# Performance work log

Hardware: AMD Instinct MI355X
Metric: run time of the kernel (lower is better)

## Reference

```python
import jax, jax.numpy as jnp
import numpy as np

VAR_W = 1.0
DIST_W = 1.0
M_VAR = 0.1
M_DIST = 1.5
IGNORE = 255
C = 16  # static upper bound on instance ids (labels 1..C; 0 = background)


def setup_inputs() -> dict:
    key = jax.random.key(0)
    ks = jax.random.split(key, 6)
    shapes = [(16, 1, 1024, 1024), (16, 1, 512, 512), (16, 1, 256, 256)]
    d = {}
    for idx, s in enumerate(shapes):
        d[f"featmap{idx}"] = jax.random.normal(ks[idx], s, dtype=jnp.float32)
        d[f"gt{idx}"] = jax.random.randint(ks[3 + idx], s, 0, C + 1, dtype=jnp.int32)
    return d


def _push_pull(feats, gts):
    B = feats[0].shape[0]
    nseg = B * (C + 1)
    b_off = (jnp.arange(B, dtype=jnp.int32) * (C + 1))[:, None]  # [B,1]

    segs, valids, ffs = [], [], []
    tot_sum = jnp.zeros((nseg,), dtype=feats[0].dtype)
    tot_cnt = jnp.zeros((nseg,), dtype=feats[0].dtype)
    # pass 1: per (batch, instance) sums / counts pooled over all scales
    for f, g in zip(feats, gts):
        ff = f.reshape(B, -1)            # [B, N_s]
        gg = g.reshape(B, -1)
        valid = (gg >= 1) & (gg <= C) & (gg < IGNORE)
        lab = jnp.where(valid, gg, 0)
        seg = (lab + b_off).reshape(-1)  # [B*N_s], segment id = b*(C+1)+label
        vf = valid.reshape(-1).astype(ff.dtype)
        tot_sum = tot_sum + jax.ops.segment_sum(jnp.where(valid, ff, 0.0).reshape(-1), seg, num_segments=nseg)
        tot_cnt = tot_cnt + jax.ops.segment_sum(vf, seg, num_segments=nseg)
        segs.append(seg); valids.append(valid); ffs.append(ff)

    mean = tot_sum / jnp.maximum(tot_cnt, 1.0)  # [nseg] per-(b,instance) mean over all scales

    # pass 2: pull loss -- per-scale mean of clamp(|x - mean| - margin_var, 0)^2, summed over scales
    pull_seg = jnp.zeros((nseg,), dtype=feats[0].dtype)
    for ff, seg, valid in zip(ffs, segs, valids):
        m_pix = mean[seg].reshape(ff.shape)
        val = jnp.where(valid, jnp.square(jnp.maximum(jnp.abs(ff - m_pix) - M_VAR, 0.0)), 0.0)
        ssum = jax.ops.segment_sum(val.reshape(-1), seg, num_segments=nseg)
        scnt = jax.ops.segment_sum(valid.reshape(-1).astype(ff.dtype), seg, num_segments=nseg)
        pull_seg = pull_seg + jnp.where(scnt > 0, ssum / jnp.maximum(scnt, 1.0), 0.0)

    present = tot_cnt.reshape(B, C + 1)[:, 1:] > 0        # [B,C]
    pull_i = pull_seg.reshape(B, C + 1)[:, 1:]            # [B,C]
    n_pull = jnp.maximum(present.sum(), 1).astype(pull_i.dtype)
    pull_loss = jnp.sum(jnp.where(present, pull_i, 0.0)) / n_pull * VAR_W

    # push loss: all ordered pairs (i,j), i!=j, both present in that batch element
    m = mean.reshape(B, C + 1)[:, 1:]                     # [B,C]
    diff = jnp.abs(m[:, :, None] - m[:, None, :])         # [B,C,C]
    pv = jnp.square(jnp.maximum(2.0 * M_DIST - diff, 0.0))
    pm = present[:, :, None] & present[:, None, :] & ~jnp.eye(C, dtype=bool)[None]
    n_push = jnp.maximum(pm.sum(), 1).astype(pv.dtype)
    push_loss = jnp.sum(jnp.where(pm, pv, 0.0)) / n_push * DIST_W

    return push_loss + pull_loss


def reference(featmap0, featmap1, featmap2, gt0, gt1, gt2):
    return _push_pull([featmap0, featmap1, featmap2], [gt0, gt1, gt2])
```

## Files before the change

kernel.cpp:

```cpp
#include <hip/hip_runtime.h>


#define NSEG 272
#define M_VAR 0.1f
#define TWO_M_DIST 3.0f

__device__ __forceinline__ void gatomic_add(float* p, float v) {
  __hip_atomic_fetch_add(p, v, __ATOMIC_RELAXED, __HIP_MEMORY_SCOPE_AGENT);
}

#define GRID_BLOCKS 1008

struct Sel {
  const float4* f; const int4* g;
  int vbase, vend, stride, scale, batch;
};

__device__ __forceinline__ Sel pick(
    int b, int t,
    const float4* f0, const int4* g0,
    const float4* f1, const int4* g1,
    const float4* f2, const int4* g2) {
  Sel s;
  if (b < 768) {
    int batch = b / 48, sub = b - batch * 48;
    s.f = f0; s.g = g0; s.scale = 0; s.batch = batch;
    s.vbase = batch * 262144 + sub * 256 + t;
    s.vend  = (batch + 1) * 262144;
    s.stride = 48 * 256;
  } else if (b < 960) {
    int lb = b - 768; int batch = lb / 12, sub = lb - batch * 12;
    s.f = f1; s.g = g1; s.scale = 1; s.batch = batch;
    s.vbase = batch * 65536 + sub * 256 + t;
    s.vend  = (batch + 1) * 65536;
    s.stride = 12 * 256;
  } else {
    int lb = b - 960; int batch = lb / 3, sub = lb - batch * 3;
    s.f = f2; s.g = g2; s.scale = 2; s.batch = batch;
    s.vbase = batch * 16384 + sub * 256 + t;
    s.vend  = (batch + 1) * 16384;
    s.stride = 3 * 256;
  }
  return s;
}

__global__ __launch_bounds__(256, 4) void pass1_kernel(
    const float4* __restrict__ f0, const int4* __restrict__ g0,
    const float4* __restrict__ f1, const int4* __restrict__ g1,
    const float4* __restrict__ f2, const int4* __restrict__ g2,
    float* __restrict__ tot_sum,
    float* __restrict__ cnt)
{
  __shared__ float2 bins[17 * 256];
  const int t = threadIdx.x;
  for (int i = t; i < 17 * 256; i += 256) bins[i] = make_float2(0.f, 0.f);
  __syncthreads();

  Sel s = pick(blockIdx.x, t, f0, g0, f1, g1, f2, g2);

  for (int v = s.vbase; v < s.vend; v += s.stride) {
    float4 fv = s.f[v];
    int4   gv = s.g[v];
    {
      int idx = (int)min((unsigned)gv.x, 16u) * 256 + t;
      float2 r = bins[idx]; bins[idx] = make_float2(r.x + fv.x, r.y + 1.f);
    }
    {
      int idx = (int)min((unsigned)gv.y, 16u) * 256 + t;
      float2 r = bins[idx]; bins[idx] = make_float2(r.x + fv.y, r.y + 1.f);
    }
    {
      int idx = (int)min((unsigned)gv.z, 16u) * 256 + t;
      float2 r = bins[idx]; bins[idx] = make_float2(r.x + fv.z, r.y + 1.f);
    }
    {
      int idx = (int)min((unsigned)gv.w, 16u) * 256 + t;
      float2 r = bins[idx]; bins[idx] = make_float2(r.x + fv.w, r.y + 1.f);
    }
  }

  for (int sh = 7; sh >= 0; --sh) {
    __syncthreads();
    int off = 1 << sh;
    for (int i = t; i < 17 * off; i += 256) {
      int l = i >> sh, tt = i & (off - 1);
      int a = l * 256 + tt;
      float2 x = bins[a], y = bins[a + off];
      bins[a] = make_float2(x.x + y.x, x.y + y.y);
    }
  }
  __syncthreads();

  if (t >= 1 && t < 17) {
    float2 r = bins[t * 256];
    if (r.y != 0.f) {
      gatomic_add(&tot_sum[s.batch * 17 + t], r.x);
      gatomic_add(&cnt[s.scale * NSEG + s.batch * 17 + t], r.y);
    }
  }
}

__global__ __launch_bounds__(256) void mean_kernel(
    const float* __restrict__ tot_sum, const float* __restrict__ cnt,
    float* __restrict__ mean, float* __restrict__ tot_cnt) {
  for (int i = threadIdx.x; i < NSEG; i += 256) {
    float c = cnt[i] + cnt[NSEG + i] + cnt[2 * NSEG + i];
    tot_cnt[i] = c;
    mean[i] = tot_sum[i] / fmaxf(c, 1.f);
  }
}

__global__ __launch_bounds__(256, 8) void pass2_kernel(
    const float4* __restrict__ f0, const int4* __restrict__ g0,
    const float4* __restrict__ f1, const int4* __restrict__ g1,
    const float4* __restrict__ f2, const int4* __restrict__ g2,
    const float* __restrict__ mean,
    float* __restrict__ pull)
{
  __shared__ float bins[17 * 256];
  __shared__ float s_mean[17];
  const int t = threadIdx.x;

  Sel s = pick(blockIdx.x, t, f0, g0, f1, g1, f2, g2);

  for (int i = t; i < 17 * 256; i += 256) bins[i] = 0.f;
  if (t < 17) s_mean[t] = mean[s.batch * 17 + t];
  __syncthreads();

  for (int v = s.vbase; v < s.vend; v += s.stride) {
    float4 fv = s.f[v];
    int4   gv = s.g[v];
    {
      int l = (int)min((unsigned)gv.x, 16u);
      float d = fmaxf(fabsf(fv.x - s_mean[l]) - M_VAR, 0.f);
      bins[l * 256 + t] += d * d;
    }
    {
      int l = (int)min((unsigned)gv.y, 16u);
      float d = fmaxf(fabsf(fv.y - s_mean[l]) - M_VAR, 0.f);
      bins[l * 256 + t] += d * d;
    }
    {
      int l = (int)min((unsigned)gv.z, 16u);
      float d = fmaxf(fabsf(fv.z - s_mean[l]) - M_VAR, 0.f);
      bins[l * 256 + t] += d * d;
    }
    {
      int l = (int)min((unsigned)gv.w, 16u);
      float d = fmaxf(fabsf(fv.w - s_mean[l]) - M_VAR, 0.f);
      bins[l * 256 + t] += d * d;
    }
  }

  for (int sh = 7; sh >= 0; --sh) {
    __syncthreads();
    int off = 1 << sh;
    for (int i = t; i < 17 * off; i += 256) {
      int l = i >> sh, tt = i & (off - 1);
      bins[l * 256 + tt] += bins[l * 256 + tt + off];
    }
  }
  __syncthreads();

  if (t >= 1 && t < 17) {
    float r = bins[t * 256];
    if (r != 0.f) gatomic_add(&pull[s.scale * NSEG + s.batch * 17 + t], r);
  }
}

__global__ __launch_bounds__(256) void finalize_kernel(
    const float* __restrict__ tot_cnt, const float* __restrict__ mean,
    const float* __restrict__ cnt, const float* __restrict__ pull,
    float* __restrict__ out) {
  __shared__ float s_mean[NSEG];
  __shared__ unsigned char s_pres[NSEG];
  const int t = threadIdx.x;
  for (int i = t; i < NSEG; i += 256) {
    s_mean[i] = mean[i];
    s_pres[i] = (tot_cnt[i] > 0.f) ? 1 : 0;
  }
  __syncthreads();

  float pull_v = 0.f, pull_n = 0.f, push_v = 0.f, push_n = 0.f;

  for (int i = t; i < NSEG; i += 256) {
    int lab = i - (i / 17) * 17;
    if (lab >= 1 && s_pres[i]) {
      float ps = 0.f;
      float c0 = cnt[i];            if (c0 > 0.f) ps += pull[i] / c0;
      float c1 = cnt[NSEG + i];     if (c1 > 0.f) ps += pull[NSEG + i] / c1;
      float c2 = cnt[2 * NSEG + i]; if (c2 > 0.f) ps += pull[2 * NSEG + i] / c2;
      pull_v += ps;
      pull_n += 1.f;
    }
  }

  {
    int b = t >> 4, ii = t & 15;
    int si = b * 17 + ii + 1;
    if (s_pres[si]) {
      float mi = s_mean[si];
      for (int j = 0; j < 16; ++j) {
        if (j == ii) continue;
        int sj = b * 17 + j + 1;
        if (s_pres[sj]) {
          float d = fmaxf(TWO_M_DIST - fabsf(mi - s_mean[sj]), 0.f);
          push_v += d * d;
          push_n += 1.f;
        }
      }
    }
  }

  #pragma unroll
  for (int o = 32; o > 0; o >>= 1) {
    pull_v += __shfl_down(pull_v, o);
    pull_n += __shfl_down(pull_n, o);
    push_v += __shfl_down(push_v, o);
    push_n += __shfl_down(push_n, o);
  }
  __shared__ float r[4][4];
  int wave = t >> 6;
  if ((t & 63) == 0) { r[wave][0] = pull_v; r[wave][1] = pull_n; r[wave][2] = push_v; r[wave][3] = push_n; }
  __syncthreads();
  if (t == 0) {
    float PV = 0, PN = 0, SV = 0, SN = 0;
    for (int w = 0; w < 4; ++w) { PV += r[w][0]; PN += r[w][1]; SV += r[w][2]; SN += r[w][3]; }
    out[0] = PV / fmaxf(PN, 1.f) + SV / fmaxf(SN, 1.f);
  }
}

extern "C" void kernel_launch(void* const* d_in, const int* in_sizes, int n_in,
                              void* d_out, int out_size, void* d_ws, size_t ws_size,
                              hipStream_t stream) {
  const float4* f0 = (const float4*)d_in[0];
  const int4*   g0 = (const int4*)  d_in[1];
  const float4* f1 = (const float4*)d_in[2];
  const int4*   g1 = (const int4*)  d_in[3];
  const float4* f2 = (const float4*)d_in[4];
  const int4*   g2 = (const int4*)  d_in[5];

  float* ws      = (float*)d_ws;
  float* tot_sum = ws;
  float* cnt     = ws + NSEG;
  float* pull    = ws + 4 * NSEG;
  float* mean    = ws + 7 * NSEG;
  float* tot_cnt = ws + 8 * NSEG;

  hipMemsetAsync(d_ws, 0, 7 * NSEG * sizeof(float), stream);
  pass1_kernel<<<GRID_BLOCKS, 256, 0, stream>>>(f0, g0, f1, g1, f2, g2, tot_sum, cnt);
  mean_kernel<<<1, 256, 0, stream>>>(tot_sum, cnt, mean, tot_cnt);
  pass2_kernel<<<GRID_BLOCKS, 256, 0, stream>>>(f0, g0, f1, g1, f2, g2, mean, pull);
  finalize_kernel<<<1, 256, 0, stream>>>(tot_cnt, mean, cnt, pull, (float*)d_out);
}
```

Before: 213.9 us.

## Replace LDS histograms with register accumulators and fuse mean/finalize kernels

Both passes now keep one register accumulator per instance label, updated with predicated adds, and reduce them with wave shuffles instead of per-thread LDS bins and a tree reduction. The loop software-prefetches the next float4/int4. The mean kernel is folded into pass2's prologue, and finalize runs in the last block, chosen by an atomic ticket counter. This removes LDS traffic and two launches, at the cost of 16 compare-selects per pixel and more register pressure.

```diff
diff --git a/kernel.cpp b/kernel.cpp
--- a/kernel.cpp
+++ b/kernel.cpp
@@ -4,17 +4,13 @@
 #define NSEG 272
 #define M_VAR 0.1f
 #define TWO_M_DIST 3.0f
+#define GRID_BLOCKS 1008
 
 __device__ __forceinline__ void gatomic_add(float* p, float v) {
   __hip_atomic_fetch_add(p, v, __ATOMIC_RELAXED, __HIP_MEMORY_SCOPE_AGENT);
 }
 
-#define GRID_BLOCKS 1008
-
-struct Sel {
-  const float4* f; const int4* g;
-  int vbase, vend, stride, scale, batch;
-};
+struct Sel { const float4* f; const int4* g; int vbase, vend, stride, scale, batch; };
 
 __device__ __forceinline__ Sel pick(
     int b, int t,
@@ -25,21 +21,15 @@
   if (b < 768) {
     int batch = b / 48, sub = b - batch * 48;
     s.f = f0; s.g = g0; s.scale = 0; s.batch = batch;
-    s.vbase = batch * 262144 + sub * 256 + t;
-    s.vend  = (batch + 1) * 262144;
-    s.stride = 48 * 256;
+    s.vbase = batch * 262144 + sub * 256 + t; s.vend = (batch + 1) * 262144; s.stride = 48 * 256;
   } else if (b < 960) {
-    int lb = b - 768; int batch = lb / 12, sub = lb - batch * 12;
+    int lb = b - 768, batch = lb / 12, sub = lb - batch * 12;
     s.f = f1; s.g = g1; s.scale = 1; s.batch = batch;
-    s.vbase = batch * 65536 + sub * 256 + t;
-    s.vend  = (batch + 1) * 65536;
-    s.stride = 12 * 256;
+    s.vbase = batch * 65536 + sub * 256 + t; s.vend = (batch + 1) * 65536; s.stride = 12 * 256;
   } else {
-    int lb = b - 960; int batch = lb / 3, sub = lb - batch * 3;
+    int lb = b - 960, batch = lb / 3, sub = lb - batch * 3;
     s.f = f2; s.g = g2; s.scale = 2; s.batch = batch;
-    s.vbase = batch * 16384 + sub * 256 + t;
-    s.vend  = (batch + 1) * 16384;
-    s.stride = 3 * 256;
+    s.vbase = batch * 16384 + sub * 256 + t; s.vend = (batch + 1) * 16384; s.stride = 3 * 256;
   }
   return s;
 }
@@ -51,133 +41,140 @@
     float* __restrict__ tot_sum,
     float* __restrict__ cnt)
 {
-  __shared__ float2 bins[17 * 256];
   const int t = threadIdx.x;
-  for (int i = t; i < 17 * 256; i += 256) bins[i] = make_float2(0.f, 0.f);
-  __syncthreads();
-
   Sel s = pick(blockIdx.x, t, f0, g0, f1, g1, f2, g2);
 
-  for (int v = s.vbase; v < s.vend; v += s.stride) {
-    float4 fv = s.f[v];
-    int4   gv = s.g[v];
-    {
-      int idx = (int)min((unsigned)gv.x, 16u) * 256 + t;
-      float2 r = bins[idx]; bins[idx] = make_float2(r.x + fv.x, r.y + 1.f);
-    }
-    {
-      int idx = (int)min((unsigned)gv.y, 16u) * 256 + t;
-      float2 r = bins[idx]; bins[idx] = make_float2(r.x + fv.y, r.y + 1.f);
-    }
-    {
-      int idx = (int)min((unsigned)gv.z, 16u) * 256 + t;
-      float2 r = bins[idx]; bins[idx] = make_float2(r.x + fv.z, r.y + 1.f);
-    }
-    {
-      int idx = (int)min((unsigned)gv.w, 16u) * 256 + t;
-      float2 r = bins[idx]; bins[idx] = make_float2(r.x + fv.w, r.y + 1.f);
-    }
-  }
-
-  for (int sh = 7; sh >= 0; --sh) {
-    __syncthreads();
-    int off = 1 << sh;
-    for (int i = t; i < 17 * off; i += 256) {
-      int l = i >> sh, tt = i & (off - 1);
-      int a = l * 256 + tt;
-      float2 x = bins[a], y = bins[a + off];
-      bins[a] = make_float2(x.x + y.x, x.y + y.y);
-    }
-  }
-  __syncthreads();
-
-  if (t >= 1 && t < 17) {
-    float2 r = bins[t * 256];
-    if (r.y != 0.f) {
-      gatomic_add(&tot_sum[s.batch * 17 + t], r.x);
-      gatomic_add(&cnt[s.scale * NSEG + s.batch * 17 + t], r.y);
-    }
-  }
-}
-
-__global__ __launch_bounds__(256) void mean_kernel(
-    const float* __restrict__ tot_sum, const float* __restrict__ cnt,
-    float* __restrict__ mean, float* __restrict__ tot_cnt) {
-  for (int i = threadIdx.x; i < NSEG; i += 256) {
-    float c = cnt[i] + cnt[NSEG + i] + cnt[2 * NSEG + i];
-    tot_cnt[i] = c;
-    mean[i] = tot_sum[i] / fmaxf(c, 1.f);
-  }
-}
-
-__global__ __launch_bounds__(256, 8) void pass2_kernel(
+  float sum[16]; int cn[16];
+  #pragma unroll
+  for (int l = 0; l < 16; ++l) { sum[l] = 0.f; cn[l] = 0; }
+
+  auto body = [&](float f, int g) {
+    #pragma unroll
+    for (int l = 0; l < 16; ++l) {
+      bool m = (g == l + 1);
+      sum[l] += m ? f : 0.f;
+      cn[l]  += m ? 1 : 0;
+    }
+  };
+
+  int v = s.vbase;
+  bool have = v < s.vend;
+  float4 fv; int4 gv;
+  if (have) { fv = s.f[v]; gv = s.g[v]; }
+  while (have) {
+    int vn = v + s.stride;
+    bool hn = vn < s.vend;
+    float4 fn; int4 gn;
+    if (hn) { fn = s.f[vn]; gn = s.g[vn]; }
+    body(fv.x, gv.x); body(fv.y, gv.y); body(fv.z, gv.z); body(fv.w, gv.w);
+    fv = fn; gv = gn; v = vn; have = hn;
+  }
+
+  #pragma unroll
+  for (int l = 0; l < 16; ++l) {
+    #pragma unroll
+    for (int o = 32; o > 0; o >>= 1) {
+      sum[l] += __shfl_down(sum[l], o);
+      cn[l]  += __shfl_down(cn[l], o);
+    }
+  }
+  __shared__ float rs[4][16];
+  __shared__ int   rc[4][16];
+  int wave = t >> 6, lane = t & 63;
+  if (lane == 0) {
+    #pragma unroll
+    for (int l = 0; l < 16; ++l) { rs[wave][l] = sum[l]; rc[wave][l] = cn[l]; }
+  }
+  __syncthreads();
+  if (t < 16) {
+    float sv = rs[0][t] + rs[1][t] + rs[2][t] + rs[3][t];
+    int   cv = rc[0][t] + rc[1][t] + rc[2][t] + rc[3][t];
+    if (cv != 0) {
+      gatomic_add(&tot_sum[s.batch * 17 + t + 1], sv);
+      gatomic_add(&cnt[s.scale * NSEG + s.batch * 17 + t + 1], (float)cv);
+    }
+  }
+}
+
+__global__ __launch_bounds__(256, 4) void pass2_kernel(
     const float4* __restrict__ f0, const int4* __restrict__ g0,
     const float4* __restrict__ f1, const int4* __restrict__ g1,
     const float4* __restrict__ f2, const int4* __restrict__ g2,
-    const float* __restrict__ mean,
-    float* __restrict__ pull)
+    const float* __restrict__ tot_sum,
+    const float* __restrict__ cnt,
+    float* __restrict__ pull,
+    int* __restrict__ counter,
+    float* __restrict__ out)
 {
-  __shared__ float bins[17 * 256];
   __shared__ float s_mean[17];
   const int t = threadIdx.x;
-
   Sel s = pick(blockIdx.x, t, f0, g0, f1, g1, f2, g2);
 
-  for (int i = t; i < 17 * 256; i += 256) bins[i] = 0.f;
-  if (t < 17) s_mean[t] = mean[s.batch * 17 + t];
-  __syncthreads();
-
-  for (int v = s.vbase; v < s.vend; v += s.stride) {
-    float4 fv = s.f[v];
-    int4   gv = s.g[v];
-    {
-      int l = (int)min((unsigned)gv.x, 16u);
-      float d = fmaxf(fabsf(fv.x - s_mean[l]) - M_VAR, 0.f);
-      bins[l * 256 + t] += d * d;
-    }
-    {
-      int l = (int)min((unsigned)gv.y, 16u);
-      float d = fmaxf(fabsf(fv.y - s_mean[l]) - M_VAR, 0.f);
-      bins[l * 256 + t] += d * d;
-    }
-    {
-      int l = (int)min((unsigned)gv.z, 16u);
-      float d = fmaxf(fabsf(fv.z - s_mean[l]) - M_VAR, 0.f);
-      bins[l * 256 + t] += d * d;
-    }
-    {
-      int l = (int)min((unsigned)gv.w, 16u);
-      float d = fmaxf(fabsf(fv.w - s_mean[l]) - M_VAR, 0.f);
-      bins[l * 256 + t] += d * d;
-    }
-  }
-
-  for (int sh = 7; sh >= 0; --sh) {
-    __syncthreads();
-    int off = 1 << sh;
-    for (int i = t; i < 17 * off; i += 256) {
-      int l = i >> sh, tt = i & (off - 1);
-      bins[l * 256 + tt] += bins[l * 256 + tt + off];
-    }
-  }
-  __syncthreads();
-
-  if (t >= 1 && t < 17) {
-    float r = bins[t * 256];
-    if (r != 0.f) gatomic_add(&pull[s.scale * NSEG + s.batch * 17 + t], r);
-  }
-}
-
-__global__ __launch_bounds__(256) void finalize_kernel(
-    const float* __restrict__ tot_cnt, const float* __restrict__ mean,
-    const float* __restrict__ cnt, const float* __restrict__ pull,
-    float* __restrict__ out) {
-  __shared__ float s_mean[NSEG];
-  __shared__ unsigned char s_pres[NSEG];
-  const int t = threadIdx.x;
+  if (t < 17) {
+    int seg = s.batch * 17 + t;
+    float c = cnt[seg] + cnt[NSEG + seg] + cnt[2 * NSEG + seg];
+    s_mean[t] = tot_sum[seg] / fmaxf(c, 1.f);
+  }
+  __syncthreads();
+
+  float acc[16];
+  #pragma unroll
+  for (int l = 0; l < 16; ++l) acc[l] = 0.f;
+
+  auto body = [&](float f, int g) {
+    unsigned gi = (unsigned)g; gi = gi > 16u ? 16u : gi;
+    float d = fmaxf(fabsf(f - s_mean[gi]) - M_VAR, 0.f);
+    float d2 = d * d;
+    #pragma unroll
+    for (int l = 0; l < 16; ++l) acc[l] += (g == l + 1) ? d2 : 0.f;
+  };
+
+  int v = s.vbase;
+  bool have = v < s.vend;
+  float4 fv; int4 gv;
+  if (have) { fv = s.f[v]; gv = s.g[v]; }
+  while (have) {
+    int vn = v + s.stride;
+    bool hn = vn < s.vend;
+    float4 fn; int4 gn;
+    if (hn) { fn = s.f[vn]; gn = s.g[vn]; }
+    body(fv.x, gv.x); body(fv.y, gv.y); body(fv.z, gv.z); body(fv.w, gv.w);
+    fv = fn; gv = gn; v = vn; have = hn;
+  }
+
+  #pragma unroll
+  for (int l = 0; l < 16; ++l) {
+    #pragma unroll
+    for (int o = 32; o > 0; o >>= 1) acc[l] += __shfl_down(acc[l], o);
+  }
+  __shared__ float rs[4][16];
+  int wave = t >> 6, lane = t & 63;
+  if (lane == 0) {
+    #pragma unroll
+    for (int l = 0; l < 16; ++l) rs[wave][l] = acc[l];
+  }
+  __syncthreads();
+  if (t < 16) {
+    float sv = rs[0][t] + rs[1][t] + rs[2][t] + rs[3][t];
+    if (sv != 0.f) gatomic_add(&pull[s.scale * NSEG + s.batch * 17 + t + 1], sv);
+  }
+
+  __threadfence();
+  __shared__ int is_last;
+  if (t == 0) {
+    int ticket = __hip_atomic_fetch_add(counter, 1, __ATOMIC_ACQ_REL, __HIP_MEMORY_SCOPE_AGENT);
+    is_last = (ticket == GRID_BLOCKS - 1) ? 1 : 0;
+  }
+  __syncthreads();
+  if (!is_last) return;
+  __threadfence();
+
+  __shared__ float fz_mean[NSEG];
+  __shared__ unsigned char fz_pres[NSEG];
   for (int i = t; i < NSEG; i += 256) {
-    s_mean[i] = mean[i];
-    s_pres[i] = (tot_cnt[i] > 0.f) ? 1 : 0;
+    float c = cnt[i] + cnt[NSEG + i] + cnt[2 * NSEG + i];
+    fz_pres[i] = (c > 0.f) ? 1 : 0;
+    fz_mean[i] = tot_sum[i] / fmaxf(c, 1.f);
   }
   __syncthreads();
 
@@ -185,7 +182,7 @@
 
   for (int i = t; i < NSEG; i += 256) {
     int lab = i - (i / 17) * 17;
-    if (lab >= 1 && s_pres[i]) {
+    if (lab >= 1 && fz_pres[i]) {
       float ps = 0.f;
       float c0 = cnt[i];            if (c0 > 0.f) ps += pull[i] / c0;
       float c1 = cnt[NSEG + i];     if (c1 > 0.f) ps += pull[NSEG + i] / c1;
@@ -194,17 +191,16 @@
       pull_n += 1.f;
     }
   }
-
   {
     int b = t >> 4, ii = t & 15;
     int si = b * 17 + ii + 1;
-    if (s_pres[si]) {
-      float mi = s_mean[si];
+    if (fz_pres[si]) {
+      float mi = fz_mean[si];
       for (int j = 0; j < 16; ++j) {
         if (j == ii) continue;
         int sj = b * 17 + j + 1;
-        if (s_pres[sj]) {
-          float d = fmaxf(TWO_M_DIST - fabsf(mi - s_mean[sj]), 0.f);
+        if (fz_pres[sj]) {
+          float d = fmaxf(TWO_M_DIST - fabsf(mi - fz_mean[sj]), 0.f);
           push_v += d * d;
           push_n += 1.f;
         }
@@ -220,8 +216,7 @@
     push_n += __shfl_down(push_n, o);
   }
   __shared__ float r[4][4];
-  int wave = t >> 6;
-  if ((t & 63) == 0) { r[wave][0] = pull_v; r[wave][1] = pull_n; r[wave][2] = push_v; r[wave][3] = push_n; }
+  if (lane == 0) { r[wave][0] = pull_v; r[wave][1] = pull_n; r[wave][2] = push_v; r[wave][3] = push_n; }
   __syncthreads();
   if (t == 0) {
     float PV = 0, PN = 0, SV = 0, SN = 0;
@@ -244,12 +239,10 @@
   float* tot_sum = ws;
   float* cnt     = ws + NSEG;
   float* pull    = ws + 4 * NSEG;
-  float* mean    = ws + 7 * NSEG;
-  float* tot_cnt = ws + 8 * NSEG;
-
-  hipMemsetAsync(d_ws, 0, 7 * NSEG * sizeof(float), stream);
+  int*   counter = (int*)(ws + 7 * NSEG);
+
+  hipMemsetAsync(d_ws, 0, (7 * NSEG + 1) * sizeof(float), stream);
   pass1_kernel<<<GRID_BLOCKS, 256, 0, stream>>>(f0, g0, f1, g1, f2, g2, tot_sum, cnt);
-  mean_kernel<<<1, 256, 0, stream>>>(tot_sum, cnt, mean, tot_cnt);
-  pass2_kernel<<<GRID_BLOCKS, 256, 0, stream>>>(f0, g0, f1, g1, f2, g2, mean, pull);
-  finalize_kernel<<<1, 256, 0, stream>>>(tot_cnt, mean, cnt, pull, (float*)d_out);
-}
+  pass2_kernel<<<GRID_BLOCKS, 256, 0, stream>>>(f0, g0, f1, g1, f2, g2, tot_sum, cnt,
+                                                pull, counter, (float*)d_out);
+}
```

Result: slower. 340.7 us (+59.2%).
